# Optimization experiments

Measured on AMD Instinct MI355X. Metric: run time of the kernel, lower is better.

## Reference

```python
import jax, jax.numpy as jnp
import numpy as np

B, S, D, H, DQ, DV = 4, 2048, 1024, 16, 64, 64

def setup_inputs() -> dict:
    key = jax.random.key(0)
    ks = jax.random.split(key, 11)
    s_in = 1.0 / np.sqrt(D)
    s_o = 1.0 / np.sqrt(H * DV)
    return {
        "query": jax.random.normal(ks[0], (B, S, D), jnp.float32),
        "key":   jax.random.normal(ks[1], (B, S, D), jnp.float32),
        "value": jax.random.normal(ks[2], (B, S, D), jnp.float32),
        "Wq_w": jax.random.normal(ks[3], (D, H * DQ), jnp.float32) * s_in,
        "Wq_b": jax.random.normal(ks[4], (H * DQ,), jnp.float32) * s_in,
        "Wk_w": jax.random.normal(ks[5], (D, H * DQ), jnp.float32) * s_in,
        "Wk_b": jax.random.normal(ks[6], (H * DQ,), jnp.float32) * s_in,
        "Wv_w": jax.random.normal(ks[7], (D, H * DV), jnp.float32) * s_in,
        "Wv_b": jax.random.normal(ks[8], (H * DV,), jnp.float32) * s_in,
        "Wo_w": jax.random.normal(ks[9], (H * DV, D), jnp.float32) * s_o,
        "Wo_b": jax.random.normal(ks[10], (D,), jnp.float32) * s_o,
    }

def reference(query, key, value, Wq_w, Wq_b, Wk_w, Wk_b, Wv_w, Wv_b, Wo_w, Wo_b):
    b, s, d = query.shape
    # chunk(h, dim=-1) + cat(dim=0) == split last dim into (h, dq) per-head slices
    q = (query @ Wq_w + Wq_b).reshape(b, s, H, DQ)  # bshq
    k = (key   @ Wk_w + Wk_b).reshape(b, s, H, DQ)
    v = (value @ Wv_w + Wv_b).reshape(b, s, H, DV)
    # NOTE: source scales by sqrt(K) where K = seq_len (query.shape[1])
    scores = jnp.einsum("bshq,bthq->bhst", q, k) / jnp.sqrt(jnp.float32(s))
    attn = jax.nn.softmax(scores, axis=-1)          # (b, h, s, s)
    out = jnp.einsum("bhst,bthv->bshv", attn, v).reshape(b, s, H * DV)
    return out @ Wo_w + Wo_b
```

## Files before the change

### kernel.cpp

```cpp
#include <hip/hip_runtime.h>
#include <hip/hip_bf16.h>
#include <cstdint>


typedef __attribute__((ext_vector_type(4))) float f32x4;
typedef __attribute__((ext_vector_type(16))) float f32x16;
typedef __attribute__((ext_vector_type(8))) short bf16x8;

#define GLB const __attribute__((address_space(1))) void*
#define LDS __attribute__((address_space(3))) void*

__device__ __forceinline__ ushort f2bf(float f) {
    uint32_t u = __builtin_bit_cast(uint32_t, f);
    u += 0x7fffu + ((u >> 16) & 1u);
    return (ushort)(u >> 16);
}

__device__ __forceinline__ uint32_t cvt_pk_bf16(float lo, float hi) {
    uint32_t r;
    asm("v_cvt_pk_bf16_f32 %0, %1, %2" : "=v"(r) : "v"(lo), "v"(hi));
    return r;
}

__device__ __forceinline__ void plswap(uint32_t& a, uint32_t& b) {
    auto r = __builtin_amdgcn_permlane32_swap(a, b, false, false);
    a = r[0];
    b = r[1];
}

__global__ void prep(const float* __restrict__ qf, const float* __restrict__ kf,
                     const float* __restrict__ vf,
                     const float* __restrict__ w0, const float* __restrict__ w1,
                     const float* __restrict__ w2, const float* __restrict__ w3,
                     ushort* __restrict__ oq, ushort* __restrict__ ok,
                     ushort* __restrict__ ov,
                     ushort* __restrict__ t0, ushort* __restrict__ t1,
                     ushort* __restrict__ t2, ushort* __restrict__ t3, int n8) {
    __shared__ float tile[64][65];
    const int y = blockIdx.y;
    if (y < 3) {
        const float* in = y == 0 ? qf : y == 1 ? kf : vf;
        ushort* out     = y == 0 ? oq : y == 1 ? ok : ov;
        for (int i = blockIdx.x * blockDim.x + threadIdx.x; i < n8; i += gridDim.x * blockDim.x) {
            const float4 a = reinterpret_cast<const float4*>(in)[2 * i];
            const float4 b = reinterpret_cast<const float4*>(in)[2 * i + 1];
            uint4 o;
            o.x = cvt_pk_bf16(a.x, a.y);
            o.y = cvt_pk_bf16(a.z, a.w);
            o.z = cvt_pk_bf16(b.x, b.y);
            o.w = cvt_pk_bf16(b.z, b.w);
            reinterpret_cast<uint4*>(out)[i] = o;
        }
    } else {
        const int x = blockIdx.x;
        const int wz = x >> 8, wy = (x >> 4) & 15, wx = x & 15;
        const float* in = wz == 0 ? w0 : wz == 1 ? w1 : wz == 2 ? w2 : w3;
        ushort* out     = wz == 0 ? t0 : wz == 1 ? t1 : wz == 2 ? t2 : t3;
        const int tx = threadIdx.x & 63, ty = threadIdx.x >> 6;
        const int nb = wx * 64, kb = wy * 64;
#pragma unroll
        for (int i = ty; i < 64; i += 4)
            tile[i][tx] = in[(size_t)(kb + i) * 1024 + nb + tx];
        __syncthreads();
#pragma unroll
        for (int i = ty; i < 64; i += 4)
            out[(size_t)(nb + i) * 1024 + kb + tx] = f2bf(tile[tx][i]);
    }
}

#define GEMM_STAGE(A_, BT_, k0, Ad, Bd)                                             \
    _Pragma("unroll")                                                               \
    for (int jj = 0; jj < 2; ++jj) {                                                \
        const int t = jj * 256 + tid;                                               \
        const int lo = (jj * 256 + (tid & ~63)) * 8;                                \
        __builtin_amdgcn_global_load_lds((GLB)(A_  + (size_t)(mb + (t >> 2)) * 1024 + (k0) + (t & 3) * 8), (LDS)((Ad) + lo), 16, 0, 0); \
        __builtin_amdgcn_global_load_lds((GLB)(BT_ + (size_t)(nb + (t >> 2)) * 1024 + (k0) + (t & 3) * 8), (LDS)((Bd) + lo), 16, 0, 0); \
    }

#define GEMM_BODY(A_, BT_, SM)                                                      \
    f32x4 acc[4][4] = {};                                                           \
    GEMM_STAGE(A_, BT_, 0, (SM), (SM) + 8192)                                       \
    __syncthreads();                                                                \
    for (int k0 = 0; k0 < 1024; k0 += 32) {                                         \
        const int cur = (k0 >> 5) & 1;                                              \
        if (k0 + 32 < 1024) {                                                       \
            GEMM_STAGE(A_, BT_, k0 + 32, (SM) + ((cur ^ 1) << 12), (SM) + 8192 + ((cur ^ 1) << 12)) \
        }                                                                           \
        const ushort* Ac = (SM) + (cur << 12);                                      \
        const ushort* Bc = (SM) + 8192 + (cur << 12);                               \
        bf16x8 af[4], bfr[4];                                                       \
        _Pragma("unroll")                                                           \
        for (int i = 0; i < 4; ++i) {                                               \
            af[i]  = *(const bf16x8*)&Ac[(wr * 64 + i * 16 + r) * 32 + g * 8];      \
            bfr[i] = *(const bf16x8*)&Bc[(wc * 64 + i * 16 + r) * 32 + g * 8];      \
        }                                                                           \
        __builtin_amdgcn_s_setprio(1);                                              \
        _Pragma("unroll")                                                           \
        for (int mi = 0; mi < 4; ++mi)                                              \
            _Pragma("unroll")                                                       \
            for (int ni = 0; ni < 4; ++ni)                                          \
                acc[mi][ni] = __builtin_amdgcn_mfma_f32_16x16x32_bf16(af[mi], bfr[ni], acc[mi][ni], 0, 0, 0); \
        __builtin_amdgcn_s_setprio(0);                                              \
        __syncthreads();                                                            \
    }

__global__ __launch_bounds__(256) void gemm_qkv(const ushort* __restrict__ qb,
                                                const ushort* __restrict__ kb,
                                                const ushort* __restrict__ vb,
                                                const ushort* __restrict__ WqT,
                                                const ushort* __restrict__ WkT,
                                                const ushort* __restrict__ WvT,
                                                const float* __restrict__ Wq_b,
                                                const float* __restrict__ Wk_b,
                                                const float* __restrict__ Wv_b,
                                                ushort* __restrict__ Qp,
                                                ushort* __restrict__ Kp,
                                                ushort* __restrict__ Vt,
                                                float qscale) {
    __shared__ ushort SMEM[16384];
    const int tid = threadIdx.x;
    const int lane = tid & 63;
    const int wave = tid >> 6, wr = wave >> 1, wc = wave & 1;
    const int r = lane & 15, g = lane >> 4;
    const int proj = blockIdx.y;
    const int id = blockIdx.x;
    const int xcd = id & 7, j = id >> 3;
    const int bx = j >> 3, by = xcd * 8 + (j & 7);
    const int mb = by * 128, nb = bx * 128;

    const ushort* A    = proj == 0 ? qb : proj == 1 ? kb : vb;
    const ushort* BT   = proj == 0 ? WqT : proj == 1 ? WkT : WvT;
    const float*  bias = proj == 0 ? Wq_b : proj == 1 ? Wk_b : Wv_b;

    GEMM_BODY(A, BT, SMEM)

    if (proj < 2) {
        const float oscale = proj == 0 ? qscale : 1.0f;
        ushort* C = proj == 0 ? Qp : Kp;
#pragma unroll
        for (int ni = 0; ni < 4; ++ni) {
            const int col = nb + wc * 64 + ni * 16 + r;
            const float bv = bias[col];
#pragma unroll
            for (int mi = 0; mi < 4; ++mi) {
                const int m0 = mb + wr * 64 + mi * 16 + g * 4;
#pragma unroll
                for (int i = 0; i < 4; ++i)
                    C[(size_t)(m0 + i) * 1024 + col] = f2bf((acc[mi][ni][i] + bv) * oscale);
            }
        }
    } else {
#pragma unroll
        for (int ni = 0; ni < 4; ++ni) {
            const int colL = wc * 64 + ni * 16 + r;
            const int x8 = (colL & 7) << 3;
            const float bv = bias[nb + colL];
#pragma unroll
            for (int mi = 0; mi < 4; ++mi) {
                const int sL = wr * 64 + mi * 16 + g * 4;
                ushort4 o;
                o.x = f2bf(acc[mi][ni][0] + bv);
                o.y = f2bf(acc[mi][ni][1] + bv);
                o.z = f2bf(acc[mi][ni][2] + bv);
                o.w = f2bf(acc[mi][ni][3] + bv);
                *(ushort4*)&SMEM[colL * 128 + (sL ^ x8)] = o;
            }
        }
        __syncthreads();
        const int b = mb >> 11;
        const int sbase = mb & 2047;
#pragma unroll
        for (int p = 0; p < 8; ++p) {
            const int colL = p * 16 + (tid >> 4);
            const int cs = tid & 15;
            const int csx = cs ^ (colL & 7);
            const uint4 v = *(const uint4*)&SMEM[colL * 128 + csx * 8];
            const int gc = nb + colL;
            const int h = gc >> 6, dv = gc & 63;
            *(uint4*)&Vt[((((size_t)(b * 16 + h)) * 64 + dv) << 11) + sbase + cs * 8] = v;
        }
    }
}

__global__ __launch_bounds__(256) void gemm_out(const ushort* __restrict__ A_,
                                                const ushort* __restrict__ BT_,
                                                const float* __restrict__ bias,
                                                float* __restrict__ Cf) {
    __shared__ ushort SMEM[16384];
    const int tid = threadIdx.x;
    const int lane = tid & 63;
    const int wave = tid >> 6, wr = wave >> 1, wc = wave & 1;
    const int r = lane & 15, g = lane >> 4;
    const int id = blockIdx.x;
    const int xcd = id & 7, j = id >> 3;
    const int bx = j >> 3, by = xcd * 8 + (j & 7);
    const int mb = by * 128, nb = bx * 128;

    GEMM_BODY(A_, BT_, SMEM)

#pragma unroll
    for (int ni = 0; ni < 4; ++ni) {
        const int col = nb + wc * 64 + ni * 16 + r;
        const float bv = bias[col];
#pragma unroll
        for (int mi = 0; mi < 4; ++mi) {
            const int m0 = mb + wr * 64 + mi * 16 + g * 4;
#pragma unroll
            for (int i = 0; i < 4; ++i)
                Cf[(size_t)(m0 + i) * 1024 + col] = acc[mi][ni][i] + bv;
        }
    }
}

__global__ __launch_bounds__(512, 4) void attn_kernel(const ushort* __restrict__ Qp,
                                                      const ushort* __restrict__ Kp,
                                                      const ushort* __restrict__ Vt,
                                                      ushort* __restrict__ AO) {
    const int tid = threadIdx.x;
    const int lane = tid & 63, wave = tid >> 6;
    const int l31 = lane & 31, hl = lane >> 5;
    const int id = blockIdx.x;
    const int xcd = id & 7, j = id >> 3;
    const int qt = j & 7;
    const int grp = xcd * 8 + (j >> 3);
    const int h = grp & 15, b = grp >> 4;
    const int qrow = qt * 256 + wave * 32 + l31;

    const ushort* Qh = Qp + (size_t)b * 2048 * 1024 + h * 64;
    const ushort* Kh = Kp + (size_t)b * 2048 * 1024 + h * 64;
    const ushort* Vh = Vt + ((size_t)(b * 16 + h)) * 64 * 2048;

    __shared__ ushort Ks[2][64 * 64];
    __shared__ ushort Vs[2][64 * 64];

    const int srow = tid >> 3;
    const int scb  = ((tid & 7) * 16) ^ ((srow & 7) << 4);
    const int wlds = wave * 512;
    const ushort* gKn = Kh + (size_t)srow * 1024 + (scb >> 1) + 64 * 1024;
    const ushort* gVn = Vh + (size_t)srow * 2048 + (scb >> 1) + 64;

    int fro2[2][4];
#pragma unroll
    for (int t2 = 0; t2 < 2; ++t2)
#pragma unroll
        for (int c = 0; c < 4; ++c) {
            const int row = t2 * 32 + l31;
            fro2[t2][c] = row * 128 + ((c * 32 + hl * 16) ^ ((row & 7) << 4));
        }

    bf16x8 qf[4];
#pragma unroll
    for (int kq = 0; kq < 4; ++kq)
        qf[kq] = *(const bf16x8*)&Qh[(size_t)qrow * 1024 + kq * 16 + hl * 8];

    f32x16 o2[2] = {};
    float ell = 0.f;

    __builtin_amdgcn_global_load_lds((GLB)(gKn - 64 * 1024), (LDS)(Ks[0] + wlds), 16, 0, 0);
    __builtin_amdgcn_global_load_lds((GLB)(gVn - 64), (LDS)(Vs[0] + wlds), 16, 0, 0);
    __syncthreads();

    for (int t0 = 0; t0 < 2048; t0 += 64) {
        const int cur = (t0 >> 6) & 1;
        if (t0 + 64 < 2048) {
            __builtin_amdgcn_global_load_lds((GLB)gKn, (LDS)(Ks[cur ^ 1] + wlds), 16, 0, 0);
            __builtin_amdgcn_global_load_lds((GLB)gVn, (LDS)(Vs[cur ^ 1] + wlds), 16, 0, 0);
            gKn += 64 * 1024;
            gVn += 64;
        }

        const char* Kb = (const char*)Ks[cur];
        const char* Vb = (const char*)Vs[cur];

        bf16x8 pfr[2][2];
#pragma unroll
        for (int th = 0; th < 2; ++th) {
            f32x16 s = {};
            __builtin_amdgcn_s_setprio(1);
#pragma unroll
            for (int kq = 0; kq < 4; ++kq) {
                const bf16x8 kf = *(const bf16x8*)(Kb + fro2[th][kq]);
                s = __builtin_amdgcn_mfma_f32_32x32x16_bf16(kf, qf[kq], s, 0, 0, 0);
            }
            __builtin_amdgcn_s_setprio(0);

            float p[16];
#pragma unroll
            for (int i = 0; i < 16; ++i) p[i] = __builtin_amdgcn_exp2f(s[i]);
            ell += ((p[0] + p[1]) + (p[2] + p[3])) + ((p[4] + p[5]) + (p[6] + p[7]))
                 + ((p[8] + p[9]) + (p[10] + p[11])) + ((p[12] + p[13]) + (p[14] + p[15]));

            uint32_t w0 = cvt_pk_bf16(p[0], p[1]);
            uint32_t w1 = cvt_pk_bf16(p[2], p[3]);
            uint32_t w2 = cvt_pk_bf16(p[4], p[5]);
            uint32_t w3 = cvt_pk_bf16(p[6], p[7]);
            plswap(w0, w2);
            plswap(w1, w3);
            uint4 f0; f0.x = w0; f0.y = w1; f0.z = w2; f0.w = w3;
            pfr[th][0] = __builtin_bit_cast(bf16x8, f0);
            uint32_t w4 = cvt_pk_bf16(p[8], p[9]);
            uint32_t w5 = cvt_pk_bf16(p[10], p[11]);
            uint32_t w6 = cvt_pk_bf16(p[12], p[13]);
            uint32_t w7 = cvt_pk_bf16(p[14], p[15]);
            plswap(w4, w6);
            plswap(w5, w7);
            uint4 f1; f1.x = w4; f1.y = w5; f1.z = w6; f1.w = w7;
            pfr[th][1] = __builtin_bit_cast(bf16x8, f1);
        }

        __builtin_amdgcn_s_setprio(1);
#pragma unroll
        for (int vh = 0; vh < 2; ++vh)
#pragma unroll
            for (int kt = 0; kt < 4; ++kt) {
                const bf16x8 vf = *(const bf16x8*)(Vb + fro2[vh][kt]);
                o2[vh] = __builtin_amdgcn_mfma_f32_32x32x16_bf16(vf, pfr[kt >> 1][kt & 1], o2[vh], 0, 0, 0);
            }
        __builtin_amdgcn_s_setprio(0);

        __syncthreads();
    }

    ell += __shfl_xor(ell, 32);
    const float inv = 1.f / ell;
#pragma unroll
    for (int vh = 0; vh < 2; ++vh)
#pragma unroll
        for (int g4 = 0; g4 < 4; ++g4) {
            ushort4 o;
            o.x = f2bf(o2[vh][4 * g4 + 0] * inv);
            o.y = f2bf(o2[vh][4 * g4 + 1] * inv);
            o.z = f2bf(o2[vh][4 * g4 + 2] * inv);
            o.w = f2bf(o2[vh][4 * g4 + 3] * inv);
            const int dvb = 8 * g4 + 4 * hl + 32 * vh;
            *(ushort4*)&AO[(size_t)(b * 2048 + qrow) * 1024 + h * 64 + dvb] = o;
        }
}

extern "C" void kernel_launch(void* const* d_in, const int* in_sizes, int n_in,
                              void* d_out, int out_size, void* d_ws, size_t ws_size,
                              hipStream_t stream) {
    const float* q_f  = (const float*)d_in[0];
    const float* k_f  = (const float*)d_in[1];
    const float* v_f  = (const float*)d_in[2];
    const float* Wq_w = (const float*)d_in[3];
    const float* Wq_b = (const float*)d_in[4];
    const float* Wk_w = (const float*)d_in[5];
    const float* Wk_b = (const float*)d_in[6];
    const float* Wv_w = (const float*)d_in[7];
    const float* Wv_b = (const float*)d_in[8];
    const float* Wo_w = (const float*)d_in[9];
    const float* Wo_b = (const float*)d_in[10];
    float* out = (float*)d_out;
    char* ws = (char*)d_ws;

    const size_t MB = 1ull << 20;
    ushort* qb  = (ushort*)(ws);
    ushort* kb  = (ushort*)(ws + 16 * MB);
    ushort* vb  = (ushort*)(ws + 32 * MB);
    ushort* WqT = (ushort*)(ws + 48 * MB);
    ushort* WkT = (ushort*)(ws + 50 * MB);
    ushort* WvT = (ushort*)(ws + 52 * MB);
    ushort* WoT = (ushort*)(ws + 54 * MB);
    ushort* Qp  = (ushort*)(ws + 56 * MB);
    ushort* Kp  = (ushort*)(ws + 72 * MB);
    ushort* Vt  = (ushort*)(ws + 88 * MB);
    ushort* AO  = qb;

    const int n8 = (4 * 2048 * 1024) / 8;
    prep<<<dim3(1024, 4), 256, 0, stream>>>(q_f, k_f, v_f, Wq_w, Wk_w, Wv_w, Wo_w,
                                            qb, kb, vb, WqT, WkT, WvT, WoT, n8);

    constexpr float QSCALE = (float)(1.4426950408889634 / 45.254833995939045);

    gemm_qkv<<<dim3(512, 3), 256, 0, stream>>>(qb, kb, vb, WqT, WkT, WvT,
                                               Wq_b, Wk_b, Wv_b, Qp, Kp, Vt, QSCALE);

    attn_kernel<<<512, 512, 0, stream>>>(Qp, Kp, Vt, AO);

    gemm_out<<<512, 256, 0, stream>>>(AO, WoT, Wo_b, out);
}
```

Baseline: 187.9 us.

## Fuse fp32-to-bf16 activation conversion into QKV GEMM A-tile loads

The separate prep pass that converted query/key/value from fp32 to bf16 is removed. The QKV GEMM now loads fp32 A tiles through registers, converts them to bf16 in-kernel and writes them to padded LDS, with the loads issued one k-step ahead of the MFMA work. This avoids a full read-write round trip of three activation tensors through global memory. The cost is twice the A-tile read bandwidth inside the GEMM, extra conversion instructions, and register-staged loads in place of the direct global-to-LDS path.

```diff
diff --git a/kernel.cpp b/kernel.cpp
--- a/kernel.cpp
+++ b/kernel.cpp
@@ -28,85 +28,28 @@
     b = r[1];
 }
 
-__global__ void prep(const float* __restrict__ qf, const float* __restrict__ kf,
-                     const float* __restrict__ vf,
-                     const float* __restrict__ w0, const float* __restrict__ w1,
+__global__ void prep(const float* __restrict__ w0, const float* __restrict__ w1,
                      const float* __restrict__ w2, const float* __restrict__ w3,
-                     ushort* __restrict__ oq, ushort* __restrict__ ok,
-                     ushort* __restrict__ ov,
                      ushort* __restrict__ t0, ushort* __restrict__ t1,
-                     ushort* __restrict__ t2, ushort* __restrict__ t3, int n8) {
+                     ushort* __restrict__ t2, ushort* __restrict__ t3) {
     __shared__ float tile[64][65];
-    const int y = blockIdx.y;
-    if (y < 3) {
-        const float* in = y == 0 ? qf : y == 1 ? kf : vf;
-        ushort* out     = y == 0 ? oq : y == 1 ? ok : ov;
-        for (int i = blockIdx.x * blockDim.x + threadIdx.x; i < n8; i += gridDim.x * blockDim.x) {
-            const float4 a = reinterpret_cast<const float4*>(in)[2 * i];
-            const float4 b = reinterpret_cast<const float4*>(in)[2 * i + 1];
-            uint4 o;
-            o.x = cvt_pk_bf16(a.x, a.y);
-            o.y = cvt_pk_bf16(a.z, a.w);
-            o.z = cvt_pk_bf16(b.x, b.y);
-            o.w = cvt_pk_bf16(b.z, b.w);
-            reinterpret_cast<uint4*>(out)[i] = o;
-        }
-    } else {
-        const int x = blockIdx.x;
-        const int wz = x >> 8, wy = (x >> 4) & 15, wx = x & 15;
-        const float* in = wz == 0 ? w0 : wz == 1 ? w1 : wz == 2 ? w2 : w3;
-        ushort* out     = wz == 0 ? t0 : wz == 1 ? t1 : wz == 2 ? t2 : t3;
-        const int tx = threadIdx.x & 63, ty = threadIdx.x >> 6;
-        const int nb = wx * 64, kb = wy * 64;
-#pragma unroll
-        for (int i = ty; i < 64; i += 4)
-            tile[i][tx] = in[(size_t)(kb + i) * 1024 + nb + tx];
-        __syncthreads();
-#pragma unroll
-        for (int i = ty; i < 64; i += 4)
-            out[(size_t)(nb + i) * 1024 + kb + tx] = f2bf(tile[tx][i]);
-    }
-}
-
-#define GEMM_STAGE(A_, BT_, k0, Ad, Bd)                                             \
-    _Pragma("unroll")                                                               \
-    for (int jj = 0; jj < 2; ++jj) {                                                \
-        const int t = jj * 256 + tid;                                               \
-        const int lo = (jj * 256 + (tid & ~63)) * 8;                                \
-        __builtin_amdgcn_global_load_lds((GLB)(A_  + (size_t)(mb + (t >> 2)) * 1024 + (k0) + (t & 3) * 8), (LDS)((Ad) + lo), 16, 0, 0); \
-        __builtin_amdgcn_global_load_lds((GLB)(BT_ + (size_t)(nb + (t >> 2)) * 1024 + (k0) + (t & 3) * 8), (LDS)((Bd) + lo), 16, 0, 0); \
-    }
-
-#define GEMM_BODY(A_, BT_, SM)                                                      \
-    f32x4 acc[4][4] = {};                                                           \
-    GEMM_STAGE(A_, BT_, 0, (SM), (SM) + 8192)                                       \
-    __syncthreads();                                                                \
-    for (int k0 = 0; k0 < 1024; k0 += 32) {                                         \
-        const int cur = (k0 >> 5) & 1;                                              \
-        if (k0 + 32 < 1024) {                                                       \
-            GEMM_STAGE(A_, BT_, k0 + 32, (SM) + ((cur ^ 1) << 12), (SM) + 8192 + ((cur ^ 1) << 12)) \
-        }                                                                           \
-        const ushort* Ac = (SM) + (cur << 12);                                      \
-        const ushort* Bc = (SM) + 8192 + (cur << 12);                               \
-        bf16x8 af[4], bfr[4];                                                       \
-        _Pragma("unroll")                                                           \
-        for (int i = 0; i < 4; ++i) {                                               \
-            af[i]  = *(const bf16x8*)&Ac[(wr * 64 + i * 16 + r) * 32 + g * 8];      \
-            bfr[i] = *(const bf16x8*)&Bc[(wc * 64 + i * 16 + r) * 32 + g * 8];      \
-        }                                                                           \
-        __builtin_amdgcn_s_setprio(1);                                              \
-        _Pragma("unroll")                                                           \
-        for (int mi = 0; mi < 4; ++mi)                                              \
-            _Pragma("unroll")                                                       \
-            for (int ni = 0; ni < 4; ++ni)                                          \
-                acc[mi][ni] = __builtin_amdgcn_mfma_f32_16x16x32_bf16(af[mi], bfr[ni], acc[mi][ni], 0, 0, 0); \
-        __builtin_amdgcn_s_setprio(0);                                              \
-        __syncthreads();                                                            \
-    }
-
-__global__ __launch_bounds__(256) void gemm_qkv(const ushort* __restrict__ qb,
-                                                const ushort* __restrict__ kb,
-                                                const ushort* __restrict__ vb,
+    const int wz = blockIdx.z, wy = blockIdx.y, wx = blockIdx.x;
+    const float* in = wz == 0 ? w0 : wz == 1 ? w1 : wz == 2 ? w2 : w3;
+    ushort* out     = wz == 0 ? t0 : wz == 1 ? t1 : wz == 2 ? t2 : t3;
+    const int tx = threadIdx.x & 63, ty = threadIdx.x >> 6;
+    const int nb = wx * 64, kb = wy * 64;
+#pragma unroll
+    for (int i = ty; i < 64; i += 4)
+        tile[i][tx] = in[(size_t)(kb + i) * 1024 + nb + tx];
+    __syncthreads();
+#pragma unroll
+    for (int i = ty; i < 64; i += 4)
+        out[(size_t)(nb + i) * 1024 + kb + tx] = f2bf(tile[tx][i]);
+}
+
+__global__ __launch_bounds__(256) void gemm_qkv(const float* __restrict__ q_f,
+                                                const float* __restrict__ k_f,
+                                                const float* __restrict__ v_f,
                                                 const ushort* __restrict__ WqT,
                                                 const ushort* __restrict__ WkT,
                                                 const ushort* __restrict__ WvT,
@@ -117,7 +60,7 @@
                                                 ushort* __restrict__ Kp,
                                                 ushort* __restrict__ Vt,
                                                 float qscale) {
-    __shared__ ushort SMEM[16384];
+    __shared__ ushort SMEM[18432];
     const int tid = threadIdx.x;
     const int lane = tid & 63;
     const int wave = tid >> 6, wr = wave >> 1, wc = wave & 1;
@@ -128,11 +71,85 @@
     const int bx = j >> 3, by = xcd * 8 + (j & 7);
     const int mb = by * 128, nb = bx * 128;
 
-    const ushort* A    = proj == 0 ? qb : proj == 1 ? kb : vb;
+    const float*  Af   = proj == 0 ? q_f : proj == 1 ? k_f : v_f;
     const ushort* BT   = proj == 0 ? WqT : proj == 1 ? WkT : WvT;
     const float*  bias = proj == 0 ? Wq_b : proj == 1 ? Wk_b : Wv_b;
 
-    GEMM_BODY(A, BT, SMEM)
+    const int arow = tid >> 1, ahalf = tid & 1;
+    const float* gA = Af + (size_t)(mb + arow) * 1024 + ahalf * 16;
+    const int awb = arow * 80 + ahalf * 32;
+
+    f32x4 acc[4][4] = {};
+
+    {
+        float4 a0 = *(const float4*)(gA + 0);
+        float4 a1 = *(const float4*)(gA + 4);
+        float4 a2 = *(const float4*)(gA + 8);
+        float4 a3 = *(const float4*)(gA + 12);
+#pragma unroll
+        for (int jj = 0; jj < 2; ++jj) {
+            const int t = jj * 256 + tid;
+            const int lo = 10240 + (jj * 256 + (tid & ~63)) * 8;
+            __builtin_amdgcn_global_load_lds((GLB)(BT + (size_t)(nb + (t >> 2)) * 1024 + (t & 3) * 8),
+                                             (LDS)(SMEM + lo), 16, 0, 0);
+        }
+        uint4 w0v, w1v;
+        w0v.x = cvt_pk_bf16(a0.x, a0.y); w0v.y = cvt_pk_bf16(a0.z, a0.w);
+        w0v.z = cvt_pk_bf16(a1.x, a1.y); w0v.w = cvt_pk_bf16(a1.z, a1.w);
+        w1v.x = cvt_pk_bf16(a2.x, a2.y); w1v.y = cvt_pk_bf16(a2.z, a2.w);
+        w1v.z = cvt_pk_bf16(a3.x, a3.y); w1v.w = cvt_pk_bf16(a3.z, a3.w);
+        *(uint4*)((char*)SMEM + awb) = w0v;
+        *(uint4*)((char*)SMEM + awb + 16) = w1v;
+    }
+    __syncthreads();
+
+    for (int k0 = 0; k0 < 1024; k0 += 32) {
+        const int cur = (k0 >> 5) & 1;
+        const bool more = (k0 + 32 < 1024);
+        float4 a0, a1, a2, a3;
+        if (more) {
+            const float* gn = gA + k0 + 32;
+            a0 = *(const float4*)(gn + 0);
+            a1 = *(const float4*)(gn + 4);
+            a2 = *(const float4*)(gn + 8);
+            a3 = *(const float4*)(gn + 12);
+#pragma unroll
+            for (int jj = 0; jj < 2; ++jj) {
+                const int t = jj * 256 + tid;
+                const int lo = 10240 + ((cur ^ 1) << 12) + (jj * 256 + (tid & ~63)) * 8;
+                __builtin_amdgcn_global_load_lds((GLB)(BT + (size_t)(nb + (t >> 2)) * 1024 + k0 + 32 + (t & 3) * 8),
+                                                 (LDS)(SMEM + lo), 16, 0, 0);
+            }
+        }
+
+        const ushort* Ac = SMEM + (cur ? 5120 : 0);
+        const ushort* Bc = SMEM + 10240 + (cur << 12);
+        bf16x8 af[4], bfr[4];
+#pragma unroll
+        for (int i = 0; i < 4; ++i) {
+            af[i]  = *(const bf16x8*)((const char*)Ac + (wr * 64 + i * 16 + r) * 80 + g * 16);
+            bfr[i] = *(const bf16x8*)&Bc[(wc * 64 + i * 16 + r) * 32 + g * 8];
+        }
+        __builtin_amdgcn_s_setprio(1);
+#pragma unroll
+        for (int mi = 0; mi < 4; ++mi)
+#pragma unroll
+            for (int ni = 0; ni < 4; ++ni)
+                acc[mi][ni] = __builtin_amdgcn_mfma_f32_16x16x32_bf16(af[mi], bfr[ni], acc[mi][ni], 0, 0, 0);
+        __builtin_amdgcn_s_setprio(0);
+
+        if (more) {
+            const int wb = (cur ? 0 : 5120 * 2) + awb;
+            uint4 w0v, w1v;
+            w0v.x = cvt_pk_bf16(a0.x, a0.y); w0v.y = cvt_pk_bf16(a0.z, a0.w);
+            w0v.z = cvt_pk_bf16(a1.x, a1.y); w0v.w = cvt_pk_bf16(a1.z, a1.w);
+            w1v.x = cvt_pk_bf16(a2.x, a2.y); w1v.y = cvt_pk_bf16(a2.z, a2.w);
+            w1v.z = cvt_pk_bf16(a3.x, a3.y); w1v.w = cvt_pk_bf16(a3.z, a3.w);
+            *(uint4*)((char*)SMEM + wb) = w0v;
+            *(uint4*)((char*)SMEM + wb + 16) = w1v;
+        }
+        __syncthreads();
+    }
 
     if (proj < 2) {
         const float oscale = proj == 0 ? qscale : 1.0f;
@@ -181,6 +198,15 @@
         }
     }
 }
+
+#define GEMM_STAGE(A_, BT_, k0, Ad, Bd)                                             \
+    _Pragma("unroll")                                                               \
+    for (int jj = 0; jj < 2; ++jj) {                                                \
+        const int t = jj * 256 + tid;                                               \
+        const int lo = (jj * 256 + (tid & ~63)) * 8;                                \
+        __builtin_amdgcn_global_load_lds((GLB)(A_  + (size_t)(mb + (t >> 2)) * 1024 + (k0) + (t & 3) * 8), (LDS)((Ad) + lo), 16, 0, 0); \
+        __builtin_amdgcn_global_load_lds((GLB)(BT_ + (size_t)(nb + (t >> 2)) * 1024 + (k0) + (t & 3) * 8), (LDS)((Bd) + lo), 16, 0, 0); \
+    }
 
 __global__ __launch_bounds__(256) void gemm_out(const ushort* __restrict__ A_,
                                                 const ushort* __restrict__ BT_,
@@ -196,7 +222,31 @@
     const int bx = j >> 3, by = xcd * 8 + (j & 7);
     const int mb = by * 128, nb = bx * 128;
 
-    GEMM_BODY(A_, BT_, SMEM)
+    f32x4 acc[4][4] = {};
+    GEMM_STAGE(A_, BT_, 0, SMEM, SMEM + 8192)
+    __syncthreads();
+    for (int k0 = 0; k0 < 1024; k0 += 32) {
+        const int cur = (k0 >> 5) & 1;
+        if (k0 + 32 < 1024) {
+            GEMM_STAGE(A_, BT_, k0 + 32, SMEM + ((cur ^ 1) << 12), SMEM + 8192 + ((cur ^ 1) << 12))
+        }
+        const ushort* Ac = SMEM + (cur << 12);
+        const ushort* Bc = SMEM + 8192 + (cur << 12);
+        bf16x8 af[4], bfr[4];
+#pragma unroll
+        for (int i = 0; i < 4; ++i) {
+            af[i]  = *(const bf16x8*)&Ac[(wr * 64 + i * 16 + r) * 32 + g * 8];
+            bfr[i] = *(const bf16x8*)&Bc[(wc * 64 + i * 16 + r) * 32 + g * 8];
+        }
+        __builtin_amdgcn_s_setprio(1);
+#pragma unroll
+        for (int mi = 0; mi < 4; ++mi)
+#pragma unroll
+            for (int ni = 0; ni < 4; ++ni)
+                acc[mi][ni] = __builtin_amdgcn_mfma_f32_16x16x32_bf16(af[mi], bfr[ni], acc[mi][ni], 0, 0, 0);
+        __builtin_amdgcn_s_setprio(0);
+        __syncthreads();
+    }
 
 #pragma unroll
     for (int ni = 0; ni < 4; ++ni) {
@@ -355,9 +405,7 @@
     char* ws = (char*)d_ws;
 
     const size_t MB = 1ull << 20;
-    ushort* qb  = (ushort*)(ws);
-    ushort* kb  = (ushort*)(ws + 16 * MB);
-    ushort* vb  = (ushort*)(ws + 32 * MB);
+    ushort* AO  = (ushort*)(ws);
     ushort* WqT = (ushort*)(ws + 48 * MB);
     ushort* WkT = (ushort*)(ws + 50 * MB);
     ushort* WvT = (ushort*)(ws + 52 * MB);
@@ -365,15 +413,13 @@
     ushort* Qp  = (ushort*)(ws + 56 * MB);
     ushort* Kp  = (ushort*)(ws + 72 * MB);
     ushort* Vt  = (ushort*)(ws + 88 * MB);
-    ushort* AO  = qb;
-
-    const int n8 = (4 * 2048 * 1024) / 8;
-    prep<<<dim3(1024, 4), 256, 0, stream>>>(q_f, k_f, v_f, Wq_w, Wk_w, Wv_w, Wo_w,
-                                            qb, kb, vb, WqT, WkT, WvT, WoT, n8);
+
+    prep<<<dim3(16, 16, 4), 256, 0, stream>>>(Wq_w, Wk_w, Wv_w, Wo_w,
+                                              WqT, WkT, WvT, WoT);
 
     constexpr float QSCALE = (float)(1.4426950408889634 / 45.254833995939045);
 
-    gemm_qkv<<<dim3(512, 3), 256, 0, stream>>>(qb, kb, vb, WqT, WkT, WvT,
+    gemm_qkv<<<dim3(512, 3), 256, 0, stream>>>(q_f, k_f, v_f, WqT, WkT, WvT,
                                                Wq_b, Wk_b, Wv_b, Qp, Kp, Vt, QSCALE);
 
     attn_kernel<<<512, 512, 0, stream>>>(Qp, Kp, Vt, AO);
```

Result: no change. 189.5 us (+0.9%).
